# Kernel optimization log

Hardware: AMD Instinct MI355X
Metric: run time of the kernel (lower is better)

Reference implementation:

```python
import jax, jax.numpy as jnp
import numpy as np

PAD = -2.0 ** 16 + 1.0  # tf code uses -2**16+1 as masked logit
ITERATIONS = 3


def squash(x):
    # x: [..., out_units]
    n = jnp.sum(jnp.square(x), axis=-1, keepdims=True)
    return (n / (1.0 + n) / jnp.sqrt(n + 1e-9)) * x


def setup_inputs() -> dict:
    key = jax.random.key(0)
    k1, k2, k3, k4 = jax.random.split(key, 4)
    B, L, DIN, DOUT, K = 4096, 200, 64, 64, 8
    return {
        "low_capsule": jax.random.normal(k1, (B, L, DIN), dtype=jnp.float32),
        "seq_len": jax.random.randint(k2, (B, 1), 1, L + 1, dtype=jnp.int32),
        "B_matrix": jax.random.normal(k3, (1, K, L), dtype=jnp.float32),
        "S_matrix": jax.random.normal(k4, (DIN, DOUT), dtype=jnp.float32),
    }


def reference(low_capsule, seq_len, B_matrix, S_matrix):
    # low_capsule: [B, L, Din]; seq_len: [B, 1]; B_matrix: [1, K, L]; S_matrix: [Din, Dout]
    L = B_matrix.shape[2]
    # tf.sequence_mask(tile(seq_len,[1,K]), L) -> [B, K, L]; K axis broadcasts.
    mask = jnp.arange(L)[None, None, :] < seq_len[:, :, None]  # [B, 1, L]
    # low_capsule_new is identical every iteration; compute once.
    low_new = jnp.einsum('bli,io->blo', low_capsule, S_matrix)  # [B, L, Dout]
    Bc = B_matrix  # routing logits, updated (stateful assign_add in tf)
    high = None
    for _ in range(ITERATIONS):
        logits = jnp.where(mask, Bc, PAD)  # [B, K, L]
        W = jax.nn.softmax(logits, axis=-1)
        high = squash(jnp.einsum('bkl,blo->bko', W, low_new))  # [B, K, Dout]
        # B_delta = sum_b high @ low_new^T, keepdims on batch
        Bc = Bc + jnp.einsum('bko,blo->kl', high, low_new)[None]  # [1, K, L]
    return high
```

## Files before the change

### kernel.cpp

```cpp
#include <hip/hip_runtime.h>
#include <math.h>


#define B_SZ  4096
#define L_SZ  200
#define DK    64
#define K_SZ  8

__device__ __forceinline__ float rl(float x, int i) {
    return __int_as_float(__builtin_amdgcn_readlane(__float_as_int(x), i));
}

__global__ __launch_bounds__(256) void k_init(const float* __restrict__ Bm,
                                              const float* __restrict__ S,
                                              float* __restrict__ Bc,
                                              float* __restrict__ St) {
    int i = blockIdx.x * 256 + threadIdx.x;
    if (i < K_SZ * L_SZ) Bc[i] = Bm[i];
    int j = i - K_SZ * L_SZ;
    if (j >= 0 && j < DK * DK) {
        int o = j >> 6, ii = j & 63;
        St[j] = S[ii * DK + o];
    }
}

__global__ __launch_bounds__(256) void k_soft(const float* __restrict__ Bc,
                                              float* __restrict__ Wt_g) {
    __shared__ float W_s[K_SZ][L_SZ];
    int t = threadIdx.x;
    int s = blockIdx.x + 1;
    int k = t >> 5, g = t & 31;

    const float* bk = Bc + k * L_SZ;
    float m = -3.4e38f;
    for (int l = g; l < s; l += 32) m = fmaxf(m, bk[l]);
    #pragma unroll
    for (int st = 16; st; st >>= 1) m = fmaxf(m, __shfl_xor(m, st, 32));
    float sum = 0.f;
    for (int l = g; l < L_SZ; l += 32) {
        float e = (l < s) ? __expf(bk[l] - m) : 0.f;
        sum += e;
        W_s[k][l] = e;
    }
    #pragma unroll
    for (int st = 16; st; st >>= 1) sum += __shfl_xor(sum, st, 32);
    float rinv = 1.0f / sum;
    for (int l = g; l < L_SZ; l += 32) W_s[k][l] *= rinv;
    __syncthreads();

    float* dst = Wt_g + (long)(s - 1) * (K_SZ * L_SZ);
    for (int j = t; j < K_SZ * L_SZ; j += 256)
        dst[j] = W_s[j & 7][j >> 3];
}

template<int WRITE_OUT>
__global__ __launch_bounds__(256, 8) void k_route4(const float* __restrict__ lc_g,
                                                   const int* __restrict__ seq_len,
                                                   const float* __restrict__ Wt_g,
                                                   const float* __restrict__ S_g,
                                                   const float* __restrict__ St_g,
                                                   float* __restrict__ partial,
                                                   float* __restrict__ out) {
    __shared__ float hp_part[4][K_SZ][DK];
    __shared__ float hp_s[K_SZ][DK];
    __shared__ float hs_s[K_SZ][DK];
    int t = threadIdx.x;
    int b = blockIdx.x;
    const float* __restrict__ lcb = lc_g + (long)b * (L_SZ * DK);
    int k = t >> 5, g = t & 31;
    int lam = t & 63;
    int w = __builtin_amdgcn_readfirstlane(t >> 6);

    int sl = seq_len[b];
    const float* __restrict__ wbase = Wt_g + (long)(sl - 1) * (K_SZ * L_SZ);

    float acc[K_SZ] = {};
    {
        const float* lp = lcb + lam;
        #pragma unroll 2
        for (int j = 0; j < 50; ++j) {
            int l = w + 4 * j;
            float v = lp[l * DK];
            const float* wr = wbase + l * K_SZ;
            acc[0] = fmaf(wr[0], v, acc[0]);
            acc[1] = fmaf(wr[1], v, acc[1]);
            acc[2] = fmaf(wr[2], v, acc[2]);
            acc[3] = fmaf(wr[3], v, acc[3]);
            acc[4] = fmaf(wr[4], v, acc[4]);
            acc[5] = fmaf(wr[5], v, acc[5]);
            acc[6] = fmaf(wr[6], v, acc[6]);
            acc[7] = fmaf(wr[7], v, acc[7]);
        }
        #pragma unroll
        for (int kk = 0; kk < K_SZ; ++kk) hp_part[w][kk][lam] = acc[kk];
    }
    __syncthreads();

    {
        int kk = t >> 5, ii = (t & 31) * 2;
        float2 r = make_float2(0.f, 0.f);
        #pragma unroll
        for (int ww = 0; ww < 4; ++ww) {
            float2 p = *(const float2*)&hp_part[ww][kk][ii];
            r.x += p.x; r.y += p.y;
        }
        *(float2*)&hp_s[kk][ii] = r;
    }
    __syncthreads();

    float h0 = 0.f, h1 = 0.f;
    {
        const float* sp = S_g + 2 * g;
        #pragma unroll 8
        for (int i = 0; i < DK; ++i) {
            float pv = hp_s[k][i];
            float2 sv = *(const float2*)(sp + i * DK);
            h0 = fmaf(pv, sv.x, h0); h1 = fmaf(pv, sv.y, h1);
        }
        float nn = h0 * h0 + h1 * h1;
        #pragma unroll
        for (int st = 16; st; st >>= 1) nn += __shfl_xor(nn, st, 32);
        float sc = nn / ((1.0f + nn) * sqrtf(nn + 1e-9f));
        h0 *= sc; h1 *= sc;
    }
    if (WRITE_OUT) {
        float2* ob2 = (float2*)(out + (long)b * (K_SZ * DK) + k * DK);
        ob2[g] = make_float2(h0, h1);
        return;
    }
    *(float2*)&hp_s[k][2 * g] = make_float2(h0, h1);

    {
        float s0 = 0.f, s1 = 0.f;
        const float* stp = St_g + 2 * g;
        #pragma unroll 8
        for (int o = 0; o < DK; ++o) {
            float hv = hp_s[k][o];
            float2 sv = *(const float2*)(stp + o * DK);
            s0 = fmaf(hv, sv.x, s0); s1 = fmaf(hv, sv.y, s1);
        }
        *(float2*)&hs_s[k][2 * g] = make_float2(s0, s1);
    }
    __syncthreads();

    float hsr[K_SZ];
    #pragma unroll
    for (int kk = 0; kk < K_SZ; ++kk) hsr[kk] = hs_s[kk][lam];
    if (t < L_SZ) {
        const float4* row4 = (const float4*)(lcb + (long)t * DK);
        float a[K_SZ] = {};
        #pragma unroll
        for (int i4 = 0; i4 < 16; ++i4) {
            float4 v = row4[i4];
            #pragma unroll
            for (int kk = 0; kk < K_SZ; ++kk) {
                a[kk] = fmaf(rl(hsr[kk], 4 * i4 + 0), v.x,
                        fmaf(rl(hsr[kk], 4 * i4 + 1), v.y,
                        fmaf(rl(hsr[kk], 4 * i4 + 2), v.z,
                        fmaf(rl(hsr[kk], 4 * i4 + 3), v.w, a[kk]))));
            }
        }
        float* pb = partial + (long)b * (K_SZ * L_SZ);
        #pragma unroll
        for (int kk = 0; kk < K_SZ; ++kk)
            pb[kk * L_SZ + t] = a[kk];
    }
}

__global__ __launch_bounds__(256) void k_reduceA(const float* __restrict__ partial,
                                                 float* __restrict__ partial2) {
    __shared__ float red[256];
    int x = blockIdx.x % 50;
    int y = blockIdx.x / 50;
    int t = threadIdx.x;
    int i = x * 32 + (t & 31);
    int sub = t >> 5;
    float s = 0.f;
    for (int p = y * 256 + sub; p < (y + 1) * 256; p += 8)
        s += partial[(long)p * (K_SZ * L_SZ) + i];
    red[t] = s;
    __syncthreads();
    for (int step = 4; step >= 1; step >>= 1) {
        if (sub < step) red[t] += red[t + step * 32];
        __syncthreads();
    }
    if (sub == 0) partial2[y * (K_SZ * L_SZ) + i] = red[t];
}

__global__ __launch_bounds__(256) void k_reduceB(const float* __restrict__ partial2,
                                                 float* __restrict__ Bc) {
    int i = blockIdx.x * 256 + threadIdx.x;
    if (i < K_SZ * L_SZ) {
        float s = 0.f;
        #pragma unroll
        for (int y = 0; y < 16; ++y) s += partial2[y * (K_SZ * L_SZ) + i];
        Bc[i] += s;
    }
}

extern "C" void kernel_launch(void* const* d_in, const int* in_sizes, int n_in,
                              void* d_out, int out_size, void* d_ws, size_t ws_size,
                              hipStream_t stream) {
    const float* lc = (const float*)d_in[0];
    const int*   sl = (const int*)d_in[1];
    const float* Bm = (const float*)d_in[2];
    const float* S  = (const float*)d_in[3];
    float* out = (float*)d_out;
    float* ws  = (float*)d_ws;

    float* Bc      = ws;
    float* St      = Bc + 1600;
    float* Wt      = St + 4096;
    float* partial = Wt + 200 * (K_SZ * L_SZ);
    float* p2      = out;

    k_init<<<23, 256, 0, stream>>>(Bm, S, Bc, St);

    k_soft     <<<200, 256, 0, stream>>>(Bc, Wt);
    k_route4<0><<<B_SZ, 256, 0, stream>>>(lc, sl, Wt, S, St, partial, out);
    k_reduceA  <<<800, 256, 0, stream>>>(partial, p2);
    k_reduceB  <<<7, 256, 0, stream>>>(p2, Bc);

    k_soft     <<<200, 256, 0, stream>>>(Bc, Wt);
    k_route4<0><<<B_SZ, 256, 0, stream>>>(lc, sl, Wt, S, St, partial, out);
    k_reduceA  <<<800, 256, 0, stream>>>(partial, p2);
    k_reduceB  <<<7, 256, 0, stream>>>(p2, Bc);

    k_soft     <<<200, 256, 0, stream>>>(Bc, Wt);
    k_route4<1><<<B_SZ, 256, 0, stream>>>(lc, sl, Wt, S, St, partial, out);
}
```

Measured before the change: 328.9 us.

## Stage softmax weights in LDS and vectorize the weighted-sum pass over capsules

The weighted sum of low capsules now first copies the per-sequence-length softmax weights into shared memory with an XOR swizzle, so they no longer come from global memory for every element. The input is then read as coalesced float4 chunks, each thread keeping eight float4 accumulators, and the partial sums are combined with wave shuffles before the existing cross-wave reduction. The softmax kernel stores weights in k-major layout with float4 copies to match the new staging. This aims to cut scalar global loads and improve memory throughput, at the cost of more registers and lower occupancy (launch bound hint drops from 8 to 6).

```diff
diff --git a/kernel.cpp b/kernel.cpp
--- a/kernel.cpp
+++ b/kernel.cpp
@@ -6,6 +6,7 @@
 #define L_SZ  200
 #define DK    64
 #define K_SZ  8
+#define KL    (K_SZ * L_SZ)
 
 __device__ __forceinline__ float rl(float x, int i) {
     return __int_as_float(__builtin_amdgcn_readlane(__float_as_int(x), i));
@@ -16,8 +17,8 @@
                                               float* __restrict__ Bc,
                                               float* __restrict__ St) {
     int i = blockIdx.x * 256 + threadIdx.x;
-    if (i < K_SZ * L_SZ) Bc[i] = Bm[i];
-    int j = i - K_SZ * L_SZ;
+    if (i < KL) Bc[i] = Bm[i];
+    int j = i - KL;
     if (j >= 0 && j < DK * DK) {
         int o = j >> 6, ii = j & 63;
         St[j] = S[ii * DK + o];
@@ -48,66 +49,110 @@
     for (int l = g; l < L_SZ; l += 32) W_s[k][l] *= rinv;
     __syncthreads();
 
-    float* dst = Wt_g + (long)(s - 1) * (K_SZ * L_SZ);
-    for (int j = t; j < K_SZ * L_SZ; j += 256)
-        dst[j] = W_s[j & 7][j >> 3];
+    float4* dst = (float4*)(Wt_g + (long)(s - 1) * KL);
+    const float4* src = (const float4*)&W_s[0][0];
+    for (int j = t; j < KL / 4; j += 256) dst[j] = src[j];
 }
 
 template<int WRITE_OUT>
-__global__ __launch_bounds__(256, 8) void k_route4(const float* __restrict__ lc_g,
+__global__ __launch_bounds__(256, 6) void k_route5(const float* __restrict__ lc_g,
                                                    const int* __restrict__ seq_len,
                                                    const float* __restrict__ Wt_g,
                                                    const float* __restrict__ S_g,
                                                    const float* __restrict__ St_g,
                                                    float* __restrict__ partial,
                                                    float* __restrict__ out) {
+    __shared__ float Wl[KL];
     __shared__ float hp_part[4][K_SZ][DK];
     __shared__ float hp_s[K_SZ][DK];
     __shared__ float hs_s[K_SZ][DK];
     int t = threadIdx.x;
     int b = blockIdx.x;
     const float* __restrict__ lcb = lc_g + (long)b * (L_SZ * DK);
+    const float4* __restrict__ lc4 = (const float4*)lcb;
+    int sl = seq_len[b];
+
+    {
+        const float* __restrict__ src = Wt_g + (long)(sl - 1) * KL;
+        for (int j = t; j < KL; j += 256) {
+            int k = j / L_SZ;
+            int l = j - k * L_SZ;
+            Wl[(l * 8 + k) ^ ((l & 3) << 2)] = src[j];
+        }
+    }
+    __syncthreads();
+
+    int grp = t >> 4;
+    int w = t >> 6;
+    float4 a[8];
+    #pragma unroll
+    for (int p = 0; p < 8; ++p) a[p] = make_float4(0.f, 0.f, 0.f, 0.f);
+
+    #pragma unroll 4
+    for (int j = 0; j < 12; ++j) {
+        float4 v = lc4[t + 256 * j];
+        int r = grp + 16 * j;
+        int c = (r & 3) << 2;
+        float4 wa = *(const float4*)&Wl[(r * 8) ^ c];
+        float4 wb = *(const float4*)&Wl[(r * 8 + 4) ^ c];
+        float wk[8] = {wa.x, wa.y, wa.z, wa.w, wb.x, wb.y, wb.z, wb.w};
+        #pragma unroll
+        for (int p = 0; p < 8; ++p) {
+            a[p].x = fmaf(wk[p], v.x, a[p].x);
+            a[p].y = fmaf(wk[p], v.y, a[p].y);
+            a[p].z = fmaf(wk[p], v.z, a[p].z);
+            a[p].w = fmaf(wk[p], v.w, a[p].w);
+        }
+    }
+    if (t < 128) {
+        float4 v = lc4[t + 3072];
+        int r = grp + 192;
+        int c = (r & 3) << 2;
+        float4 wa = *(const float4*)&Wl[(r * 8) ^ c];
+        float4 wb = *(const float4*)&Wl[(r * 8 + 4) ^ c];
+        float wk[8] = {wa.x, wa.y, wa.z, wa.w, wb.x, wb.y, wb.z, wb.w};
+        #pragma unroll
+        for (int p = 0; p < 8; ++p) {
+            a[p].x = fmaf(wk[p], v.x, a[p].x);
+            a[p].y = fmaf(wk[p], v.y, a[p].y);
+            a[p].z = fmaf(wk[p], v.z, a[p].z);
+            a[p].w = fmaf(wk[p], v.w, a[p].w);
+        }
+    }
+
+    #pragma unroll
+    for (int p = 0; p < 8; ++p) {
+        a[p].x += __shfl_xor(a[p].x, 16, 64);
+        a[p].y += __shfl_xor(a[p].y, 16, 64);
+        a[p].z += __shfl_xor(a[p].z, 16, 64);
+        a[p].w += __shfl_xor(a[p].w, 16, 64);
+        a[p].x += __shfl_xor(a[p].x, 32, 64);
+        a[p].y += __shfl_xor(a[p].y, 32, 64);
+        a[p].z += __shfl_xor(a[p].z, 32, 64);
+        a[p].w += __shfl_xor(a[p].w, 32, 64);
+    }
+    if ((t & 63) < 16) {
+        int c0 = (t & 15) * 4;
+        #pragma unroll
+        for (int p = 0; p < 8; ++p)
+            *(float4*)&hp_part[w][p][c0] = a[p];
+    }
+    __syncthreads();
+
+    {
+        int kk = t >> 5, ii = (t & 31) * 2;
+        float2 r2 = make_float2(0.f, 0.f);
+        #pragma unroll
+        for (int ww = 0; ww < 4; ++ww) {
+            float2 p = *(const float2*)&hp_part[ww][kk][ii];
+            r2.x += p.x; r2.y += p.y;
+        }
+        *(float2*)&hp_s[kk][ii] = r2;
+    }
+    __syncthreads();
+
     int k = t >> 5, g = t & 31;
     int lam = t & 63;
-    int w = __builtin_amdgcn_readfirstlane(t >> 6);
-
-    int sl = seq_len[b];
-    const float* __restrict__ wbase = Wt_g + (long)(sl - 1) * (K_SZ * L_SZ);
-
-    float acc[K_SZ] = {};
-    {
-        const float* lp = lcb + lam;
-        #pragma unroll 2
-        for (int j = 0; j < 50; ++j) {
-            int l = w + 4 * j;
-            float v = lp[l * DK];
-            const float* wr = wbase + l * K_SZ;
-            acc[0] = fmaf(wr[0], v, acc[0]);
-            acc[1] = fmaf(wr[1], v, acc[1]);
-            acc[2] = fmaf(wr[2], v, acc[2]);
-            acc[3] = fmaf(wr[3], v, acc[3]);
-            acc[4] = fmaf(wr[4], v, acc[4]);
-            acc[5] = fmaf(wr[5], v, acc[5]);
-            acc[6] = fmaf(wr[6], v, acc[6]);
-            acc[7] = fmaf(wr[7], v, acc[7]);
-        }
-        #pragma unroll
-        for (int kk = 0; kk < K_SZ; ++kk) hp_part[w][kk][lam] = acc[kk];
-    }
-    __syncthreads();
-
-    {
-        int kk = t >> 5, ii = (t & 31) * 2;
-        float2 r = make_float2(0.f, 0.f);
-        #pragma unroll
-        for (int ww = 0; ww < 4; ++ww) {
-            float2 p = *(const float2*)&hp_part[ww][kk][ii];
-            r.x += p.x; r.y += p.y;
-        }
-        *(float2*)&hp_s[kk][ii] = r;
-    }
-    __syncthreads();
-
     float h0 = 0.f, h1 = 0.f;
     {
         const float* sp = S_g + 2 * g;
@@ -148,22 +193,22 @@
     for (int kk = 0; kk < K_SZ; ++kk) hsr[kk] = hs_s[kk][lam];
     if (t < L_SZ) {
         const float4* row4 = (const float4*)(lcb + (long)t * DK);
-        float a[K_SZ] = {};
+        float aa[K_SZ] = {};
         #pragma unroll
         for (int i4 = 0; i4 < 16; ++i4) {
             float4 v = row4[i4];
             #pragma unroll
             for (int kk = 0; kk < K_SZ; ++kk) {
-                a[kk] = fmaf(rl(hsr[kk], 4 * i4 + 0), v.x,
-                        fmaf(rl(hsr[kk], 4 * i4 + 1), v.y,
-                        fmaf(rl(hsr[kk], 4 * i4 + 2), v.z,
-                        fmaf(rl(hsr[kk], 4 * i4 + 3), v.w, a[kk]))));
+                aa[kk] = fmaf(rl(hsr[kk], 4 * i4 + 0), v.x,
+                         fmaf(rl(hsr[kk], 4 * i4 + 1), v.y,
+                         fmaf(rl(hsr[kk], 4 * i4 + 2), v.z,
+                         fmaf(rl(hsr[kk], 4 * i4 + 3), v.w, aa[kk]))));
             }
         }
-        float* pb = partial + (long)b * (K_SZ * L_SZ);
+        float* pb = partial + (long)b * KL;
         #pragma unroll
         for (int kk = 0; kk < K_SZ; ++kk)
-            pb[kk * L_SZ + t] = a[kk];
+            pb[kk * L_SZ + t] = aa[kk];
     }
 }
 
@@ -177,23 +222,23 @@
     int sub = t >> 5;
     float s = 0.f;
     for (int p = y * 256 + sub; p < (y + 1) * 256; p += 8)
-        s += partial[(long)p * (K_SZ * L_SZ) + i];
+        s += partial[(long)p * KL + i];
     red[t] = s;
     __syncthreads();
     for (int step = 4; step >= 1; step >>= 1) {
         if (sub < step) red[t] += red[t + step * 32];
         __syncthreads();
     }
-    if (sub == 0) partial2[y * (K_SZ * L_SZ) + i] = red[t];
+    if (sub == 0) partial2[y * KL + i] = red[t];
 }
 
 __global__ __launch_bounds__(256) void k_reduceB(const float* __restrict__ partial2,
                                                  float* __restrict__ Bc) {
     int i = blockIdx.x * 256 + threadIdx.x;
-    if (i < K_SZ * L_SZ) {
+    if (i < KL) {
         float s = 0.f;
         #pragma unroll
-        for (int y = 0; y < 16; ++y) s += partial2[y * (K_SZ * L_SZ) + i];
+        for (int y = 0; y < 16; ++y) s += partial2[y * KL + i];
         Bc[i] += s;
     }
 }
@@ -211,21 +256,21 @@
     float* Bc      = ws;
     float* St      = Bc + 1600;
     float* Wt      = St + 4096;
-    float* partial = Wt + 200 * (K_SZ * L_SZ);
+    float* partial = Wt + 200 * KL;
     float* p2      = out;
 
     k_init<<<23, 256, 0, stream>>>(Bm, S, Bc, St);
 
     k_soft     <<<200, 256, 0, stream>>>(Bc, Wt);
-    k_route4<0><<<B_SZ, 256, 0, stream>>>(lc, sl, Wt, S, St, partial, out);
+    k_route5<0><<<B_SZ, 256, 0, stream>>>(lc, sl, Wt, S, St, partial, out);
     k_reduceA  <<<800, 256, 0, stream>>>(partial, p2);
     k_reduceB  <<<7, 256, 0, stream>>>(p2, Bc);
 
     k_soft     <<<200, 256, 0, stream>>>(Bc, Wt);
-    k_route4<0><<<B_SZ, 256, 0, stream>>>(lc, sl, Wt, S, St, partial, out);
+    k_route5<0><<<B_SZ, 256, 0, stream>>>(lc, sl, Wt, S, St, partial, out);
     k_reduceA  <<<800, 256, 0, stream>>>(partial, p2);
     k_reduceB  <<<7, 256, 0, stream>>>(p2, Bc);
 
     k_soft     <<<200, 256, 0, stream>>>(Bc, Wt);
-    k_route4<1><<<B_SZ, 256, 0, stream>>>(lc, sl, Wt, S, St, partial, out);
-}
+    k_route5<1><<<B_SZ, 256, 0, stream>>>(lc, sl, Wt, S, St, partial, out);
+}
```

Result: faster. 312.6 us (-5.0%).
